# Kernel tuning notes

Hardware: AMD Instinct MI355X
Metric: run time of the kernel (lower is better)

## Reference

```python
import jax, jax.numpy as jnp
import numpy as np

WS = 8
NH = 8


def setup_inputs() -> dict:
    key = jax.random.key(0)
    ks = jax.random.split(key, 5)
    B, H, W, C = 4, 256, 256, 256
    x = jax.random.normal(ks[0], (B, H * W, C), dtype=jnp.float32)
    qkv_w = jax.random.normal(ks[1], (3 * C, C), dtype=jnp.float32) * (C ** -0.5)
    proj_w = jax.random.normal(ks[2], (C, C), dtype=jnp.float32) * (C ** -0.5)
    proj_b = jnp.zeros((C,), dtype=jnp.float32)
    bias = jax.random.normal(ks[3], (NH, WS * WS, WS * WS), dtype=jnp.float32) * 0.02
    return {"x": x, "qkv_w": qkv_w, "proj_w": proj_w, "proj_b": proj_b,
            "bias": bias, "H": H, "W": W}


def reference(x, qkv_w, proj_w, proj_b, bias, H, W):
    B, L, C = x.shape
    hd = C // NH
    scale = hd ** -0.5
    pad_r = (WS - W % WS) % WS
    pad_b = (WS - H % WS) % WS
    xv = x.reshape(B, H, W, C)
    if pad_r > 0 or pad_b > 0:
        xv = jnp.pad(xv, ((0, 0), (0, pad_b), (0, pad_r), (0, 0)))
    Hp, Wp = H + pad_b, W + pad_r
    nHw, nWw = Hp // WS, Wp // WS
    # window partition -> [B*nHw*nWw, WS*WS, C]
    xw = (xv.reshape(B, nHw, WS, nWw, WS, C)
            .transpose(0, 1, 3, 2, 4, 5)
            .reshape(-1, WS * WS, C))
    # qkv: [nw, t, 3C] -> [3, nw, nh, t, hd]
    qkv = jnp.einsum('ntc,dc->ntd', xw, qkv_w)
    qkv = qkv.reshape(-1, WS * WS, 3, NH, hd).transpose(2, 0, 3, 1, 4)
    q, k, v = qkv[0], qkv[1], qkv[2]
    attn = jnp.einsum('whqd,whkd->whqk', q * scale, k) + bias[None]
    out = jnp.einsum('whqk,whkd->whqd', jax.nn.softmax(attn, axis=-1), v)
    out = out.transpose(0, 2, 1, 3).reshape(-1, WS * WS, C)
    out = jnp.einsum('ntc,dc->ntd', out, proj_w) + proj_b
    # reverse window partition
    out = (out.reshape(B, nHw, nWw, WS, WS, C)
              .transpose(0, 1, 3, 2, 4, 5)
              .reshape(B, Hp, Wp, C))
    if pad_r > 0 or pad_b > 0:
        out = out[:, :H, :W, :]
    return out.reshape(B, L, C)
```

## Files before the change

### kernel.cpp

```cpp
#include <hip/hip_runtime.h>

typedef unsigned short u16;
typedef __bf16 bf16x8 __attribute__((ext_vector_type(8)));
typedef float f32x4 __attribute__((ext_vector_type(4)));

#define MFMA(a, b, c) __builtin_amdgcn_mfma_f32_16x16x32_bf16(a, b, c, 0, 0, 0)

static __device__ __forceinline__ u16 f2bf(float f) {
  unsigned u = __float_as_uint(f);
  u = u + 0x7FFFu + ((u >> 16) & 1u);
  return (u16)(u >> 16);
}

static __device__ __forceinline__ f32x4 fzero() {
  f32x4 z; z[0] = 0.f; z[1] = 0.f; z[2] = 0.f; z[3] = 0.f; return z;
}

__global__ void cvt_w(const float* __restrict__ qw, const float* __restrict__ pw,
                      u16* __restrict__ o) {
  int i = blockIdx.x * 256 + threadIdx.x;
  float v = (i < 196608) ? qw[i] : pw[i - 196608];
  o[i] = f2bf(v);
}

__global__ __launch_bounds__(256, 2) void swin(
    const float* __restrict__ x, const u16* __restrict__ wqkv,
    const u16* __restrict__ wproj, const float* __restrict__ pb,
    const float* __restrict__ bias, float* __restrict__ out) {

  __shared__ u16 Xs[64 * 264];
  __shared__ u16 QK[2][2][64 * 40];
  __shared__ u16 Vt[2][32 * 72];

  const int tid  = threadIdx.x;
  const int wv   = tid >> 6;
  const int lane = tid & 63;
  const int l15  = lane & 15;
  const int quad = lane >> 4;

  const int w  = blockIdx.x;
  const int bb = w >> 10;
  const int wh = (w >> 5) & 31;
  const int ww = w & 31;

  {
    const float* xb = x + ((size_t)bb << 24);
    #pragma unroll
    for (int i = 0; i < 16; ++i) {
      int flat = i * 256 + tid;
      int t  = flat >> 6;
      int c4 = flat & 63;
      int row = wh * 8 + (t >> 3), col = ww * 8 + (t & 7);
      const float4 v = *(const float4*)(xb + ((size_t)(row * 256 + col) << 8) + c4 * 4);
      unsigned p0 = (unsigned)f2bf(v.x) | ((unsigned)f2bf(v.y) << 16);
      unsigned p1 = (unsigned)f2bf(v.z) | ((unsigned)f2bf(v.w) << 16);
      *(uint2*)&Xs[t * 264 + c4 * 4] = make_uint2(p0, p1);
    }
  }
  __syncthreads();

  const float scale = 0.17677669529663687f;
  unsigned opk[4][8];

  #pragma unroll
  for (int s = 0; s < 4; ++s) {
    {
      f32x4 acc[3][4];
      #pragma unroll
      for (int a = 0; a < 3; ++a)
        #pragma unroll
        for (int m = 0; m < 4; ++m) acc[a][m] = fzero();

      #pragma unroll
      for (int kk = 0; kk < 8; ++kk) {
        bf16x8 af[4];
        #pragma unroll
        for (int m = 0; m < 4; ++m)
          af[m] = *(const bf16x8*)&Xs[(m * 16 + l15) * 264 + kk * 32 + quad * 8];
        #pragma unroll
        for (int nt = 0; nt < 3; ++nt) {
          int j = wv * 3 + nt;
          int hl = j / 6, r = j % 6, ty = r >> 1, sub = r & 1;
          int d = ty * 256 + (2 * s + hl) * 32 + sub * 16;
          bf16x8 bf = *(const bf16x8*)(wqkv + (size_t)(d + l15) * 256 + kk * 32 + quad * 8);
          #pragma unroll
          for (int m = 0; m < 4; ++m) acc[nt][m] = MFMA(af[m], bf, acc[nt][m]);
        }
      }
      #pragma unroll
      for (int nt = 0; nt < 3; ++nt) {
        int j = wv * 3 + nt;
        int hl = j / 6, r = j % 6, ty = r >> 1, sub = r & 1;
        int dl = sub * 16 + l15;
        #pragma unroll
        for (int m = 0; m < 4; ++m) {
          if (ty == 2) {
            int t0 = m * 16 + quad * 4;
            unsigned p0 = (unsigned)f2bf(acc[nt][m][0]) | ((unsigned)f2bf(acc[nt][m][1]) << 16);
            unsigned p1 = (unsigned)f2bf(acc[nt][m][2]) | ((unsigned)f2bf(acc[nt][m][3]) << 16);
            *(uint2*)&Vt[hl][dl * 72 + t0] = make_uint2(p0, p1);
          } else {
            #pragma unroll
            for (int e = 0; e < 4; ++e) {
              int t = m * 16 + quad * 4 + e;
              QK[hl][ty][t * 40 + dl] = f2bf(acc[nt][m][e]);
            }
          }
        }
      }
    }
    __syncthreads();

    const int hl = wv >> 1, half = wv & 1;
    const int h  = 2 * s + hl;
    float sb[2][4][4];
    {
      f32x4 sacc[2][4];
      #pragma unroll
      for (int m = 0; m < 2; ++m)
        #pragma unroll
        for (int n = 0; n < 4; ++n) sacc[m][n] = fzero();
      bf16x8 qa[2];
      #pragma unroll
      for (int m = 0; m < 2; ++m) {
        int tq = (2 * half + m) * 16 + l15;
        qa[m] = *(const bf16x8*)&QK[hl][0][tq * 40 + quad * 8];
      }
      #pragma unroll
      for (int n = 0; n < 4; ++n) {
        int tk = n * 16 + l15;
        bf16x8 kb = *(const bf16x8*)&QK[hl][1][tk * 40 + quad * 8];
        #pragma unroll
        for (int m = 0; m < 2; ++m) sacc[m][n] = MFMA(qa[m], kb, sacc[m][n]);
      }
      const float* bh = bias + h * 4096;
      #pragma unroll
      for (int m = 0; m < 2; ++m)
        #pragma unroll
        for (int n = 0; n < 4; ++n)
          #pragma unroll
          for (int e = 0; e < 4; ++e) {
            int tq = (2 * half + m) * 16 + quad * 4 + e;
            int tk = n * 16 + l15;
            sb[m][n][e] = sacc[m][n][e] * scale + bh[tq * 64 + tk];
          }
    }
    float rinv[2][4];
    #pragma unroll
    for (int m = 0; m < 2; ++m)
      #pragma unroll
      for (int e = 0; e < 4; ++e) {
        float mx = sb[m][0][e];
        #pragma unroll
        for (int n = 1; n < 4; ++n) mx = fmaxf(mx, sb[m][n][e]);
        #pragma unroll
        for (int dd = 1; dd < 16; dd <<= 1) mx = fmaxf(mx, __shfl_xor(mx, dd, 64));
        float sum = 0.f;
        #pragma unroll
        for (int n = 0; n < 4; ++n) {
          float p = __expf(sb[m][n][e] - mx);
          sb[m][n][e] = p; sum += p;
        }
        #pragma unroll
        for (int dd = 1; dd < 16; dd <<= 1) sum += __shfl_xor(sum, dd, 64);
        rinv[m][e] = 1.0f / sum;
      }
    __syncthreads();

    u16* Ps = &QK[0][0][0] + hl * 4608;
    #pragma unroll
    for (int m = 0; m < 2; ++m)
      #pragma unroll
      for (int n = 0; n < 4; ++n)
        #pragma unroll
        for (int e = 0; e < 4; ++e) {
          int tq = (2 * half + m) * 16 + quad * 4 + e;
          Ps[tq * 72 + n * 16 + l15] = f2bf(sb[m][n][e]);
        }
    __syncthreads();

    {
      f32x4 oacc[2][2];
      #pragma unroll
      for (int m = 0; m < 2; ++m)
        #pragma unroll
        for (int n = 0; n < 2; ++n) oacc[m][n] = fzero();
      #pragma unroll
      for (int kk = 0; kk < 2; ++kk) {
        bf16x8 pa[2];
        #pragma unroll
        for (int m = 0; m < 2; ++m) {
          int tq = (2 * half + m) * 16 + l15;
          pa[m] = *(const bf16x8*)&Ps[tq * 72 + kk * 32 + quad * 8];
        }
        #pragma unroll
        for (int n = 0; n < 2; ++n) {
          bf16x8 vb = *(const bf16x8*)&Vt[hl][(n * 16 + l15) * 72 + kk * 32 + quad * 8];
          #pragma unroll
          for (int m = 0; m < 2; ++m) oacc[m][n] = MFMA(pa[m], vb, oacc[m][n]);
        }
      }
      #pragma unroll
      for (int m = 0; m < 2; ++m)
        #pragma unroll
        for (int n = 0; n < 2; ++n) {
          f32x4 v = oacc[m][n];
          opk[s][(m * 2 + n) * 2 + 0] =
              (unsigned)f2bf(v[0] * rinv[m][0]) | ((unsigned)f2bf(v[1] * rinv[m][1]) << 16);
          opk[s][(m * 2 + n) * 2 + 1] =
              (unsigned)f2bf(v[2] * rinv[m][2]) | ((unsigned)f2bf(v[3] * rinv[m][3]) << 16);
        }
    }
    __syncthreads();
  }

  u16* Os = Xs;
  #pragma unroll
  for (int s = 0; s < 4; ++s) {
    int h = 2 * s + (wv >> 1);
    #pragma unroll
    for (int m = 0; m < 2; ++m)
      #pragma unroll
      for (int n = 0; n < 2; ++n) {
        unsigned p0 = opk[s][(m * 2 + n) * 2 + 0];
        unsigned p1 = opk[s][(m * 2 + n) * 2 + 1];
        int ch = h * 32 + n * 16 + l15;
        int t0 = (2 * (wv & 1) + m) * 16 + quad * 4;
        Os[(t0 + 0) * 264 + ch] = (u16)(p0 & 0xFFFF);
        Os[(t0 + 1) * 264 + ch] = (u16)(p0 >> 16);
        Os[(t0 + 2) * 264 + ch] = (u16)(p1 & 0xFFFF);
        Os[(t0 + 3) * 264 + ch] = (u16)(p1 >> 16);
      }
  }
  __syncthreads();

  {
    f32x4 pacc[4][4];
    #pragma unroll
    for (int m = 0; m < 4; ++m)
      #pragma unroll
      for (int n = 0; n < 4; ++n) pacc[m][n] = fzero();
    const int n0 = wv * 64;
    #pragma unroll
    for (int kk = 0; kk < 8; ++kk) {
      bf16x8 af[4];
      #pragma unroll
      for (int m = 0; m < 4; ++m)
        af[m] = *(const bf16x8*)&Os[(m * 16 + l15) * 264 + kk * 32 + quad * 8];
      #pragma unroll
      for (int n = 0; n < 4; ++n) {
        bf16x8 bf = *(const bf16x8*)(wproj + (size_t)(n0 + n * 16 + l15) * 256 + kk * 32 + quad * 8);
        #pragma unroll
        for (int m = 0; m < 4; ++m) pacc[m][n] = MFMA(af[m], bf, pacc[m][n]);
      }
    }
    float* ob = out + ((size_t)bb << 24);
    #pragma unroll
    for (int n = 0; n < 4; ++n) {
      float bv = pb[n0 + n * 16 + l15];
      #pragma unroll
      for (int m = 0; m < 4; ++m)
        #pragma unroll
        for (int e = 0; e < 4; ++e) {
          int t = m * 16 + quad * 4 + e;
          int row = wh * 8 + (t >> 3), col = ww * 8 + (t & 7);
          ob[((size_t)(row * 256 + col) << 8) + n0 + n * 16 + l15] = pacc[m][n][e] + bv;
        }
    }
  }
}

extern "C" void kernel_launch(void* const* d_in, const int* in_sizes, int n_in,
                              void* d_out, int out_size, void* d_ws, size_t ws_size,
                              hipStream_t stream) {
  const float* x  = (const float*)d_in[0];
  const float* qw = (const float*)d_in[1];
  const float* pw = (const float*)d_in[2];
  const float* pb = (const float*)d_in[3];
  const float* bs = (const float*)d_in[4];
  u16* wbf = (u16*)d_ws;

  cvt_w<<<1024, 256, 0, stream>>>(qw, pw, wbf);
  swin<<<4096, 256, 0, stream>>>(x, wbf, wbf + 196608, pb, bs, (float*)d_out);
}
```

Measured before the change: 741.9 us.

## Rewrite Swin window-attention kernel with 512 threads, swizzled LDS, folded scale and bf16 bias

Rewrites the fused window-attention kernel to use 8 waves per block instead of 4. LDS tiles now use XOR-swizzled layouts in place of padding, which shrinks shared memory and targets bank conflicts. The attention scale is folded into the Q weights during conversion, and the bias is pre-transposed to bf16 in the weight-conversion kernel. The code also uses hardware packed bf16 conversion, one fewer barrier per head pair, and swapped MFMA operand order so softmax reductions need fewer shuffles. This trades extra preprocessing and bf16 rounding of the bias for lower register pressure, higher occupancy and less LDS traffic.

```diff
diff --git a/kernel.cpp b/kernel.cpp
--- a/kernel.cpp
+++ b/kernel.cpp
@@ -2,269 +2,237 @@
 
 typedef unsigned short u16;
 typedef __bf16 bf16x8 __attribute__((ext_vector_type(8)));
+typedef __bf16 bf16x2 __attribute__((ext_vector_type(2)));
 typedef float f32x4 __attribute__((ext_vector_type(4)));
 
-#define MFMA(a, b, c) __builtin_amdgcn_mfma_f32_16x16x32_bf16(a, b, c, 0, 0, 0)
-
-static __device__ __forceinline__ u16 f2bf(float f) {
+#define MFMA(a,b,c) __builtin_amdgcn_mfma_f32_16x16x32_bf16(a,b,c,0,0,0)
+
+static __device__ __forceinline__ u16 f2bf(float f){
   unsigned u = __float_as_uint(f);
-  u = u + 0x7FFFu + ((u >> 16) & 1u);
-  return (u16)(u >> 16);
-}
-
-static __device__ __forceinline__ f32x4 fzero() {
-  f32x4 z; z[0] = 0.f; z[1] = 0.f; z[2] = 0.f; z[3] = 0.f; return z;
+  u = u + 0x7FFFu + ((u>>16)&1u);
+  return (u16)(u>>16);
+}
+
+static __device__ __forceinline__ unsigned pk2(float a, float b){
+#if __has_builtin(__builtin_amdgcn_cvt_pk_bf16_f32)
+  bf16x2 v = __builtin_amdgcn_cvt_pk_bf16_f32(a,b);
+  return __builtin_bit_cast(unsigned, v);
+#else
+  return (unsigned)f2bf(a) | ((unsigned)f2bf(b)<<16);
+#endif
+}
+
+static __device__ __forceinline__ float bfbits2f(unsigned b){
+  return __uint_as_float(b<<16);
+}
+
+static __device__ __forceinline__ f32x4 fzero(){
+  f32x4 z; z[0]=0.f; z[1]=0.f; z[2]=0.f; z[3]=0.f; return z;
 }
 
 __global__ void cvt_w(const float* __restrict__ qw, const float* __restrict__ pw,
-                      u16* __restrict__ o) {
-  int i = blockIdx.x * 256 + threadIdx.x;
-  float v = (i < 196608) ? qw[i] : pw[i - 196608];
+                      const float* __restrict__ bias, u16* __restrict__ o){
+  int i = blockIdx.x*512 + threadIdx.x;
+  float v;
+  if (i < 196608) { v = qw[i]; if (i < 65536) v *= 0.17677669529663687f; }
+  else if (i < 262144) v = pw[i-196608];
+  else { int bi = i-262144; int h = bi>>12, k = (bi>>6)&63, q = bi&63;
+         v = bias[(h<<12)+(q<<6)+k]; }
   o[i] = f2bf(v);
 }
 
-__global__ __launch_bounds__(256, 2) void swin(
+__global__ __launch_bounds__(512,4) void swin(
     const float* __restrict__ x, const u16* __restrict__ wqkv,
     const u16* __restrict__ wproj, const float* __restrict__ pb,
-    const float* __restrict__ bias, float* __restrict__ out) {
-
-  __shared__ u16 Xs[64 * 264];
-  __shared__ u16 QK[2][2][64 * 40];
-  __shared__ u16 Vt[2][32 * 72];
-
-  const int tid  = threadIdx.x;
-  const int wv   = tid >> 6;
-  const int lane = tid & 63;
-  const int l15  = lane & 15;
-  const int quad = lane >> 4;
-
-  const int w  = blockIdx.x;
-  const int bb = w >> 10;
-  const int wh = (w >> 5) & 31;
-  const int ww = w & 31;
+    const u16* __restrict__ biasT, float* __restrict__ out){
+
+  __shared__ u16 Xs[64*256];
+  __shared__ u16 QKs[8192];
+  __shared__ u16 Vts[4096];
+
+  const int tid = threadIdx.x;
+  const int wv = tid>>6, lane = tid&63, l15 = lane&15, quad = lane>>4;
+  const int w = blockIdx.x, bb = w>>10, wh = (w>>5)&31, ww = w&31;
+  const size_t obase = ((size_t)bb)<<24;
 
   {
-    const float* xb = x + ((size_t)bb << 24);
-    #pragma unroll
-    for (int i = 0; i < 16; ++i) {
-      int flat = i * 256 + tid;
-      int t  = flat >> 6;
-      int c4 = flat & 63;
-      int row = wh * 8 + (t >> 3), col = ww * 8 + (t & 7);
-      const float4 v = *(const float4*)(xb + ((size_t)(row * 256 + col) << 8) + c4 * 4);
-      unsigned p0 = (unsigned)f2bf(v.x) | ((unsigned)f2bf(v.y) << 16);
-      unsigned p1 = (unsigned)f2bf(v.z) | ((unsigned)f2bf(v.w) << 16);
-      *(uint2*)&Xs[t * 264 + c4 * 4] = make_uint2(p0, p1);
+    const float* xb = x + obase;
+    #pragma unroll
+    for (int i = 0; i < 8; ++i) {
+      int t = i*8 + wv;
+      int c4 = lane;
+      int pix = (wh*8 + (t>>3))*256 + ww*8 + (t&7);
+      const float4 v = *(const float4*)(xb + (size_t)pix*256 + c4*4);
+      unsigned lo = pk2(v.x, v.y), hi = pk2(v.z, v.w);
+      int addr = t*256 + ((((c4>>1)^(t&7))<<3)) + (c4&1)*4;
+      *(uint2*)&Xs[addr] = make_uint2(lo,hi);
     }
   }
   __syncthreads();
 
-  const float scale = 0.17677669529663687f;
-  unsigned opk[4][8];
+  const int th = wv&1, dg = wv>>1;
+  int base0[3], hlj[3], tyj[3], dtj[3], isv[3];
+  #pragma unroll
+  for (int jl = 0; jl < 3; ++jl) {
+    int j = dg*3 + jl, hl = j/6, r = j%6, ty = r>>1, dt = r&1;
+    hlj[jl]=hl; tyj[jl]=ty; dtj[jl]=dt; isv[jl]=(ty==2);
+    base0[jl] = ty*256 + hl*32 + dt*16;
+  }
+  const int hl_a = wv>>2, qt = wv&3;
+  const int q = qt*16 + l15;
+  const int x7 = l15&7;
+
+  unsigned opkA[4][2], opkB[4][2];
 
   #pragma unroll
   for (int s = 0; s < 4; ++s) {
     {
-      f32x4 acc[3][4];
-      #pragma unroll
-      for (int a = 0; a < 3; ++a)
-        #pragma unroll
-        for (int m = 0; m < 4; ++m) acc[a][m] = fzero();
-
+      f32x4 acc[3][2];
+      #pragma unroll
+      for (int a = 0; a < 3; ++a){ acc[a][0]=fzero(); acc[a][1]=fzero(); }
+      const u16* wp0 = wqkv + (size_t)(base0[0] + s*64 + l15)*256 + quad*8;
+      const u16* wp1 = wqkv + (size_t)(base0[1] + s*64 + l15)*256 + quad*8;
+      const u16* wp2 = wqkv + (size_t)(base0[2] + s*64 + l15)*256 + quad*8;
+      const int tr0 = (2*th)*16 + l15, tr1 = tr0 + 16;
       #pragma unroll
       for (int kk = 0; kk < 8; ++kk) {
-        bf16x8 af[4];
-        #pragma unroll
-        for (int m = 0; m < 4; ++m)
-          af[m] = *(const bf16x8*)&Xs[(m * 16 + l15) * 264 + kk * 32 + quad * 8];
-        #pragma unroll
-        for (int nt = 0; nt < 3; ++nt) {
-          int j = wv * 3 + nt;
-          int hl = j / 6, r = j % 6, ty = r >> 1, sub = r & 1;
-          int d = ty * 256 + (2 * s + hl) * 32 + sub * 16;
-          bf16x8 bf = *(const bf16x8*)(wqkv + (size_t)(d + l15) * 256 + kk * 32 + quad * 8);
-          #pragma unroll
-          for (int m = 0; m < 4; ++m) acc[nt][m] = MFMA(af[m], bf, acc[nt][m]);
-        }
-      }
-      #pragma unroll
-      for (int nt = 0; nt < 3; ++nt) {
-        int j = wv * 3 + nt;
-        int hl = j / 6, r = j % 6, ty = r >> 1, sub = r & 1;
-        int dl = sub * 16 + l15;
-        #pragma unroll
-        for (int m = 0; m < 4; ++m) {
-          if (ty == 2) {
-            int t0 = m * 16 + quad * 4;
-            unsigned p0 = (unsigned)f2bf(acc[nt][m][0]) | ((unsigned)f2bf(acc[nt][m][1]) << 16);
-            unsigned p1 = (unsigned)f2bf(acc[nt][m][2]) | ((unsigned)f2bf(acc[nt][m][3]) << 16);
-            *(uint2*)&Vt[hl][dl * 72 + t0] = make_uint2(p0, p1);
+        int off = (((kk*4+quad)^x7)<<3);
+        bf16x8 xf0 = *(const bf16x8*)&Xs[tr0*256 + off];
+        bf16x8 xf1 = *(const bf16x8*)&Xs[tr1*256 + off];
+        bf16x8 wf0 = *(const bf16x8*)wp0; wp0 += 32;
+        bf16x8 wf1 = *(const bf16x8*)wp1; wp1 += 32;
+        bf16x8 wf2 = *(const bf16x8*)wp2; wp2 += 32;
+        if (isv[0]) { acc[0][0]=MFMA(xf0,wf0,acc[0][0]); acc[0][1]=MFMA(xf1,wf0,acc[0][1]); }
+        else        { acc[0][0]=MFMA(wf0,xf0,acc[0][0]); acc[0][1]=MFMA(wf0,xf1,acc[0][1]); }
+        if (isv[1]) { acc[1][0]=MFMA(xf0,wf1,acc[1][0]); acc[1][1]=MFMA(xf1,wf1,acc[1][1]); }
+        else        { acc[1][0]=MFMA(wf1,xf0,acc[1][0]); acc[1][1]=MFMA(wf1,xf1,acc[1][1]); }
+        if (isv[2]) { acc[2][0]=MFMA(xf0,wf2,acc[2][0]); acc[2][1]=MFMA(xf1,wf2,acc[2][1]); }
+        else        { acc[2][0]=MFMA(wf2,xf0,acc[2][0]); acc[2][1]=MFMA(wf2,xf1,acc[2][1]); }
+      }
+      #pragma unroll
+      for (int jl = 0; jl < 3; ++jl)
+        #pragma unroll
+        for (int tl = 0; tl < 2; ++tl) {
+          f32x4 a = acc[jl][tl];
+          unsigned lo = pk2(a[0],a[1]), hi = pk2(a[2],a[3]);
+          if (!isv[jl]) {
+            int t = (2*th+tl)*16 + l15;
+            int d0 = dtj[jl]*16 + quad*4;
+            int addr = hlj[jl]*4096 + tyj[jl]*2048 + t*32 + (((d0>>3)^(t&3))<<3) + (d0&7);
+            *(uint2*)&QKs[addr] = make_uint2(lo,hi);
           } else {
-            #pragma unroll
-            for (int e = 0; e < 4; ++e) {
-              int t = m * 16 + quad * 4 + e;
-              QK[hl][ty][t * 40 + dl] = f2bf(acc[nt][m][e]);
-            }
+            int d = dtj[jl]*16 + l15;
+            int t0 = (2*th+tl)*16 + quad*4;
+            int addr = hlj[jl]*2048 + d*64 + (((t0>>3)^(d&7))<<3) + (t0&7);
+            *(uint2*)&Vts[addr] = make_uint2(lo,hi);
           }
         }
-      }
     }
     __syncthreads();
 
-    const int hl = wv >> 1, half = wv & 1;
-    const int h  = 2 * s + hl;
-    float sb[2][4][4];
+    u16* Ph = &QKs[hl_a*4096];
+    const u16* Kh = Ph + 2048;
+    float sv[4][4]; float rinv;
     {
-      f32x4 sacc[2][4];
-      #pragma unroll
-      for (int m = 0; m < 2; ++m)
-        #pragma unroll
-        for (int n = 0; n < 4; ++n) sacc[m][n] = fzero();
-      bf16x8 qa[2];
-      #pragma unroll
-      for (int m = 0; m < 2; ++m) {
-        int tq = (2 * half + m) * 16 + l15;
-        qa[m] = *(const bf16x8*)&QK[hl][0][tq * 40 + quad * 8];
-      }
-      #pragma unroll
-      for (int n = 0; n < 4; ++n) {
-        int tk = n * 16 + l15;
-        bf16x8 kb = *(const bf16x8*)&QK[hl][1][tk * 40 + quad * 8];
-        #pragma unroll
-        for (int m = 0; m < 2; ++m) sacc[m][n] = MFMA(qa[m], kb, sacc[m][n]);
-      }
-      const float* bh = bias + h * 4096;
-      #pragma unroll
-      for (int m = 0; m < 2; ++m)
-        #pragma unroll
-        for (int n = 0; n < 4; ++n)
-          #pragma unroll
-          for (int e = 0; e < 4; ++e) {
-            int tq = (2 * half + m) * 16 + quad * 4 + e;
-            int tk = n * 16 + l15;
-            sb[m][n][e] = sacc[m][n][e] * scale + bh[tq * 64 + tk];
-          }
-    }
-    float rinv[2][4];
-    #pragma unroll
-    for (int m = 0; m < 2; ++m)
-      #pragma unroll
-      for (int e = 0; e < 4; ++e) {
-        float mx = sb[m][0][e];
-        #pragma unroll
-        for (int n = 1; n < 4; ++n) mx = fmaxf(mx, sb[m][n][e]);
-        #pragma unroll
-        for (int dd = 1; dd < 16; dd <<= 1) mx = fmaxf(mx, __shfl_xor(mx, dd, 64));
-        float sum = 0.f;
-        #pragma unroll
-        for (int n = 0; n < 4; ++n) {
-          float p = __expf(sb[m][n][e] - mx);
-          sb[m][n][e] = p; sum += p;
-        }
-        #pragma unroll
-        for (int dd = 1; dd < 16; dd <<= 1) sum += __shfl_xor(sum, dd, 64);
-        rinv[m][e] = 1.0f / sum;
-      }
+      bf16x8 qf = *(const bf16x8*)&Ph[q*32 + ((quad^(q&3))<<3)];
+      f32x4 sacc[4];
+      #pragma unroll
+      for (int mt = 0; mt < 4; ++mt) {
+        int kt = mt*16 + l15;
+        bf16x8 kf = *(const bf16x8*)&Kh[kt*32 + ((quad^(kt&3))<<3)];
+        sacc[mt] = MFMA(kf, qf, fzero());
+      }
+      const u16* bT = biasT + (2*s + hl_a)*4096 + qt*16 + l15;
+      float mx = -3.4e38f;
+      #pragma unroll
+      for (int mt = 0; mt < 4; ++mt)
+        #pragma unroll
+        for (int e = 0; e < 4; ++e) {
+          float v = sacc[mt][e] + bfbits2f(bT[(mt*16 + quad*4 + e)*64]);
+          sv[mt][e] = v; mx = fmaxf(mx, v);
+        }
+      mx = fmaxf(mx, __shfl_xor(mx, 16, 64));
+      mx = fmaxf(mx, __shfl_xor(mx, 32, 64));
+      float sum = 0.f;
+      #pragma unroll
+      for (int mt = 0; mt < 4; ++mt)
+        #pragma unroll
+        for (int e = 0; e < 4; ++e) { float p = __expf(sv[mt][e]-mx); sv[mt][e]=p; sum+=p; }
+      sum += __shfl_xor(sum, 16, 64);
+      sum += __shfl_xor(sum, 32, 64);
+      rinv = 1.0f / sum;
+    }
     __syncthreads();
 
-    u16* Ps = &QK[0][0][0] + hl * 4608;
-    #pragma unroll
-    for (int m = 0; m < 2; ++m)
-      #pragma unroll
-      for (int n = 0; n < 4; ++n)
+    #pragma unroll
+    for (int mt = 0; mt < 4; ++mt) {
+      int k0 = mt*16 + quad*4;
+      unsigned lo = pk2(sv[mt][0],sv[mt][1]), hi = pk2(sv[mt][2],sv[mt][3]);
+      int addr = q*64 + (((k0>>3)^(q&7))<<3) + (k0&7);
+      *(uint2*)&Ph[addr] = make_uint2(lo,hi);
+    }
+    {
+      const u16* Vh = &Vts[hl_a*2048];
+      f32x4 oacc[2]; oacc[0]=fzero(); oacc[1]=fzero();
+      #pragma unroll
+      for (int kk = 0; kk < 2; ++kk) {
+        bf16x8 pf = *(const bf16x8*)&Ph[q*64 + (((kk*4+quad)^(q&7))<<3)];
+        #pragma unroll
+        for (int dt = 0; dt < 2; ++dt) {
+          int d = dt*16 + l15;
+          bf16x8 vf = *(const bf16x8*)&Vh[d*64 + (((kk*4+quad)^(d&7))<<3)];
+          oacc[dt] = MFMA(vf, pf, oacc[dt]);
+        }
+      }
+      #pragma unroll
+      for (int dt = 0; dt < 2; ++dt) {
+        opkA[s][dt] = pk2(oacc[dt][0]*rinv, oacc[dt][1]*rinv);
+        opkB[s][dt] = pk2(oacc[dt][2]*rinv, oacc[dt][3]*rinv);
+      }
+    }
+    if (s == 3) {
+      #pragma unroll
+      for (int s2 = 0; s2 < 4; ++s2)
+        #pragma unroll
+        for (int dt = 0; dt < 2; ++dt) {
+          int ch = (2*s2 + hl_a)*32 + dt*16 + quad*4;
+          int addr = q*256 + (((ch>>3)^(q&7))<<3) + (ch&7);
+          *(uint2*)&Xs[addr] = make_uint2(opkA[s2][dt], opkB[s2][dt]);
+        }
+    }
+    __syncthreads();
+  }
+
+  {
+    f32x4 pacc[4][2];
+    #pragma unroll
+    for (int m = 0; m < 4; ++m){ pacc[m][0]=fzero(); pacc[m][1]=fzero(); }
+    const u16* wpA = wproj + (size_t)(wv*32 + l15)*256 + quad*8;
+    const u16* wpB = wpA + 16*256;
+    #pragma unroll
+    for (int kk = 0; kk < 8; ++kk) {
+      bf16x8 b0 = *(const bf16x8*)wpA; wpA += 32;
+      bf16x8 b1 = *(const bf16x8*)wpB; wpB += 32;
+      #pragma unroll
+      for (int m = 0; m < 4; ++m) {
+        int t = m*16 + l15;
+        bf16x8 af = *(const bf16x8*)&Xs[t*256 + (((kk*4+quad)^(t&7))<<3)];
+        pacc[m][0] = MFMA(af, b0, pacc[m][0]);
+        pacc[m][1] = MFMA(af, b1, pacc[m][1]);
+      }
+    }
+    float* ob = out + obase;
+    #pragma unroll
+    for (int n = 0; n < 2; ++n) {
+      int dout = wv*32 + n*16 + l15;
+      float bv = pb[dout];
+      #pragma unroll
+      for (int m = 0; m < 4; ++m)
         #pragma unroll
         for (int e = 0; e < 4; ++e) {
-          int tq = (2 * half + m) * 16 + quad * 4 + e;
-          Ps[tq * 72 + n * 16 + l15] = f2bf(sb[m][n][e]);
-        }
-    __syncthreads();
-
-    {
-      f32x4 oacc[2][2];
-      #pragma unroll
-      for (int m = 0; m < 2; ++m)
-        #pragma unroll
-        for (int n = 0; n < 2; ++n) oacc[m][n] = fzero();
-      #pragma unroll
-      for (int kk = 0; kk < 2; ++kk) {
-        bf16x8 pa[2];
-        #pragma unroll
-        for (int m = 0; m < 2; ++m) {
-          int tq = (2 * half + m) * 16 + l15;
-          pa[m] = *(const bf16x8*)&Ps[tq * 72 + kk * 32 + quad * 8];
-        }
-        #pragma unroll
-        for (int n = 0; n < 2; ++n) {
-          bf16x8 vb = *(const bf16x8*)&Vt[hl][(n * 16 + l15) * 72 + kk * 32 + quad * 8];
-          #pragma unroll
-          for (int m = 0; m < 2; ++m) oacc[m][n] = MFMA(pa[m], vb, oacc[m][n]);
-        }
-      }
-      #pragma unroll
-      for (int m = 0; m < 2; ++m)
-        #pragma unroll
-        for (int n = 0; n < 2; ++n) {
-          f32x4 v = oacc[m][n];
-          opk[s][(m * 2 + n) * 2 + 0] =
-              (unsigned)f2bf(v[0] * rinv[m][0]) | ((unsigned)f2bf(v[1] * rinv[m][1]) << 16);
-          opk[s][(m * 2 + n) * 2 + 1] =
-              (unsigned)f2bf(v[2] * rinv[m][2]) | ((unsigned)f2bf(v[3] * rinv[m][3]) << 16);
-        }
-    }
-    __syncthreads();
-  }
-
-  u16* Os = Xs;
-  #pragma unroll
-  for (int s = 0; s < 4; ++s) {
-    int h = 2 * s + (wv >> 1);
-    #pragma unroll
-    for (int m = 0; m < 2; ++m)
-      #pragma unroll
-      for (int n = 0; n < 2; ++n) {
-        unsigned p0 = opk[s][(m * 2 + n) * 2 + 0];
-        unsigned p1 = opk[s][(m * 2 + n) * 2 + 1];
-        int ch = h * 32 + n * 16 + l15;
-        int t0 = (2 * (wv & 1) + m) * 16 + quad * 4;
-        Os[(t0 + 0) * 264 + ch] = (u16)(p0 & 0xFFFF);
-        Os[(t0 + 1) * 264 + ch] = (u16)(p0 >> 16);
-        Os[(t0 + 2) * 264 + ch] = (u16)(p1 & 0xFFFF);
-        Os[(t0 + 3) * 264 + ch] = (u16)(p1 >> 16);
-      }
-  }
-  __syncthreads();
-
-  {
-    f32x4 pacc[4][4];
-    #pragma unroll
-    for (int m = 0; m < 4; ++m)
-      #pragma unroll
-      for (int n = 0; n < 4; ++n) pacc[m][n] = fzero();
-    const int n0 = wv * 64;
-    #pragma unroll
-    for (int kk = 0; kk < 8; ++kk) {
-      bf16x8 af[4];
-      #pragma unroll
-      for (int m = 0; m < 4; ++m)
-        af[m] = *(const bf16x8*)&Os[(m * 16 + l15) * 264 + kk * 32 + quad * 8];
-      #pragma unroll
-      for (int n = 0; n < 4; ++n) {
-        bf16x8 bf = *(const bf16x8*)(wproj + (size_t)(n0 + n * 16 + l15) * 256 + kk * 32 + quad * 8);
-        #pragma unroll
-        for (int m = 0; m < 4; ++m) pacc[m][n] = MFMA(af[m], bf, pacc[m][n]);
-      }
-    }
-    float* ob = out + ((size_t)bb << 24);
-    #pragma unroll
-    for (int n = 0; n < 4; ++n) {
-      float bv = pb[n0 + n * 16 + l15];
-      #pragma unroll
-      for (int m = 0; m < 4; ++m)
-        #pragma unroll
-        for (int e = 0; e < 4; ++e) {
-          int t = m * 16 + quad * 4 + e;
-          int row = wh * 8 + (t >> 3), col = ww * 8 + (t & 7);
-          ob[((size_t)(row * 256 + col) << 8) + n0 + n * 16 + l15] = pacc[m][n][e] + bv;
+          int t = m*16 + quad*4 + e;
+          int pix = (wh*8 + (t>>3))*256 + ww*8 + (t&7);
+          ob[(size_t)pix*256 + dout] = pacc[m][n][e] + bv;
         }
     }
   }
@@ -280,6 +248,6 @@
   const float* bs = (const float*)d_in[4];
   u16* wbf = (u16*)d_ws;
 
-  cvt_w<<<1024, 256, 0, stream>>>(qw, pw, wbf);
-  swin<<<4096, 256, 0, stream>>>(x, wbf, wbf + 196608, pb, bs, (float*)d_out);
-}
+  cvt_w<<<576, 512, 0, stream>>>(qw, pw, bs, wbf);
+  swin<<<4096, 512, 0, stream>>>(x, wbf, wbf + 196608, pb, wbf + 262144, (float*)d_out);
+}
```

New measurement: 1.019 ms. 1.37x slower.
